# Optimization experiments

Measured on AMD Instinct MI355X. Metric: run time of the kernel, lower is better.

## Reference

```python
import jax, jax.numpy as jnp
import numpy as np

D_MODEL = 1024
D_FF = 4096
N_EXPERTS = 8
TOP_K = 2
GATE_TEMP = 1.0
LOAD_BALANCE_WEIGHT = 0.01


def setup_inputs() -> dict:
    key = jax.random.key(0)
    ks = jax.random.split(key, 6)
    B, S = 4, 2048
    x = jax.random.normal(ks[0], (B, S, D_MODEL), dtype=jnp.float32)
    # gate: nn.Linear(d_model, n_experts, bias=False), weight ~ N(0, 0.1)
    gate_w = 0.1 * jax.random.normal(ks[1], (N_EXPERTS, D_MODEL), dtype=jnp.float32)
    # stacked expert weights (stored as [in, out] for x @ W)
    s1 = 1.0 / np.sqrt(D_MODEL)
    s2 = 1.0 / np.sqrt(D_FF)
    W1 = jax.random.uniform(ks[2], (N_EXPERTS, D_MODEL, D_FF), jnp.float32, -s1, s1)
    b1 = jax.random.uniform(ks[3], (N_EXPERTS, D_FF), jnp.float32, -s1, s1)
    W2 = jax.random.uniform(ks[4], (N_EXPERTS, D_FF, D_MODEL), jnp.float32, -s2, s2)
    b2 = jax.random.uniform(ks[5], (N_EXPERTS, D_MODEL), jnp.float32, -s2, s2)
    return {"x": x, "gate_w": gate_w, "W1": W1, "b1": b1, "W2": W2, "b2": b2}


def reference(x, gate_w, W1, b1, W2, b2):
    B, S, D = x.shape
    E = gate_w.shape[0]
    xf = x.reshape(-1, D)                                  # [N, D]
    logits = (xf @ gate_w.T) / GATE_TEMP                   # [N, E]
    gate_probs = jax.nn.softmax(logits, axis=-1)           # [N, E]
    topk_probs, topk_idx = jax.lax.top_k(gate_probs, TOP_K)
    topk_probs = topk_probs / jnp.sum(topk_probs, axis=-1, keepdims=True)
    # per-token combine weight for each expert: [N, E]
    combine = jnp.einsum("nk,nke->ne", topk_probs,
                         jax.nn.one_hot(topk_idx, E, dtype=xf.dtype))
    out = jnp.zeros_like(xf)
    for e in range(E):  # fixed small loop over experts (structurally distinct weights)
        h = jax.nn.gelu(xf @ W1[e] + b1[e], approximate=False)  # [N, d_ff]
        out = out + combine[:, e:e + 1] * (h @ W2[e] + b2[e])
    out = out.reshape(B, S, D)
    # auxiliary load-balance loss (faithful: softmax probs > 0 almost surely)
    prob_mean = jnp.mean(gate_probs, axis=0)
    tokens_per_expert = jnp.mean((gate_probs > 0).astype(xf.dtype), axis=0)
    aux_loss = jnp.sum(prob_mean * tokens_per_expert) * E * LOAD_BALANCE_WEIGHT
    return out, aux_loss
```

## Files before the change

kernel.cpp:

```cpp
#include <hip/hip_runtime.h>
#include <cstdint>

typedef unsigned short u16;
typedef __attribute__((ext_vector_type(8))) __bf16 bf16x8;
typedef __attribute__((ext_vector_type(4))) float f32x4;

#define NTOK 8192
#define DM   1024
#define DFF  4096
#define NE   8
#define NT_MAX256 72

typedef const __attribute__((address_space(1))) unsigned gl_u32;
typedef __attribute__((address_space(3))) unsigned lds_u32;

static __device__ __forceinline__ u16 f2bf(float f) {
    union { float f; unsigned u; } v; v.f = f;
    unsigned r = v.u + 0x7fffu + ((v.u >> 16) & 1u);
    return (u16)(r >> 16);
}

__global__ __launch_bounds__(256) void transpose_cvt_kernel(const float* __restrict__ W,
                                                            u16* __restrict__ WT,
                                                            int K, int F) {
    __shared__ float tile[64][33];
    size_t eo = (size_t)blockIdx.z * K * F;
    const float* src = W + eo;
    u16* dst = WT + eo;
    int k0 = blockIdx.y * 64, f0 = blockIdx.x * 32;
    int tid = threadIdx.x;
    {
        int rk = tid >> 2, cf = (tid & 3) * 8;
        const float* s = src + (size_t)(k0 + rk) * F + f0 + cf;
        f32x4 v0 = *(const f32x4*)(s);
        f32x4 v1 = *(const f32x4*)(s + 4);
#pragma unroll
        for (int i = 0; i < 4; i++) { tile[rk][cf + i] = v0[i]; tile[rk][cf + 4 + i] = v1[i]; }
    }
    __syncthreads();
    {
        int f = tid >> 3, kq = (tid & 7) * 8;
        union { ushort4 h[2]; uint4 q; } o;
#pragma unroll
        for (int i = 0; i < 8; i++) {
            u16 b = f2bf(tile[kq + i][f]);
            ((u16*)&o)[i] = b;
        }
        *(uint4*)(dst + (size_t)(f0 + f) * K + k0 + kq) = o.q;
    }
}

__global__ __launch_bounds__(256) void gate_kernel(const float* __restrict__ x,
                                                   const float* __restrict__ gw,
                                                   u16* __restrict__ xb,
                                                   int* __restrict__ cnt,
                                                   float* __restrict__ psum,
                                                   float* __restrict__ indsum,
                                                   int* __restrict__ list,
                                                   float* __restrict__ wgt,
                                                   int4* __restrict__ tokIE,
                                                   float2* __restrict__ tokW) {
    __shared__ float s_psum[NE], s_ind[NE];
    __shared__ int s_cnt[NE], s_base[NE];
    __shared__ int s_tok[NE][32];
    __shared__ float s_wgt[NE][32];
    __shared__ int s_e1[32], s_p1[32], s_e2[32], s_p2[32];
    __shared__ float s_w1[32], s_w2[32];
    int tid = threadIdx.x, lane = tid & 63, wid = tid >> 6;
    if (tid < NE) { s_psum[tid] = 0.f; s_ind[tid] = 0.f; s_cnt[tid] = 0; }
    __syncthreads();
#pragma unroll 1
    for (int it = 0; it < 8; it++) {
        int t = blockIdx.x * 32 + wid * 8 + it;
        const float* xr = x + (size_t)t * DM;
        float xv[16];
#pragma unroll
        for (int i = 0; i < 4; i++) {
            f32x4 v = *(const f32x4*)(xr + i * 256 + lane * 4);
            xv[4 * i + 0] = v[0]; xv[4 * i + 1] = v[1];
            xv[4 * i + 2] = v[2]; xv[4 * i + 3] = v[3];
            ushort4 o;
            o.x = f2bf(v[0]); o.y = f2bf(v[1]); o.z = f2bf(v[2]); o.w = f2bf(v[3]);
            *(ushort4*)(xb + (size_t)t * DM + i * 256 + lane * 4) = o;
        }
        float p[NE];
#pragma unroll
        for (int e = 0; e < NE; e++) {
            const float* gr = gw + (size_t)e * DM;
            float d = 0.f;
#pragma unroll
            for (int i = 0; i < 4; i++) {
                f32x4 g = *(const f32x4*)(gr + i * 256 + lane * 4);
                d += xv[4 * i] * g[0] + xv[4 * i + 1] * g[1]
                   + xv[4 * i + 2] * g[2] + xv[4 * i + 3] * g[3];
            }
#pragma unroll
            for (int off = 32; off; off >>= 1) d += __shfl_xor(d, off);
            p[e] = d;
        }
        float m = p[0];
#pragma unroll
        for (int e = 1; e < NE; e++) m = fmaxf(m, p[e]);
        float s = 0.f;
#pragma unroll
        for (int e = 0; e < NE; e++) { p[e] = expf(p[e] - m); s += p[e]; }
        float inv = 1.f / s;
#pragma unroll
        for (int e = 0; e < NE; e++) p[e] *= inv;
        int i1 = 0; float p1 = p[0];
#pragma unroll
        for (int e = 1; e < NE; e++) if (p[e] > p1) { p1 = p[e]; i1 = e; }
        int i2 = (i1 == 0) ? 1 : 0; float p2 = p[i2];
#pragma unroll
        for (int e = 0; e < NE; e++) if (e != i1 && p[e] > p2) { p2 = p[e]; i2 = e; }
        float wnorm = 1.f / (p1 + p2);
        if (lane == 0) {
#pragma unroll
            for (int e = 0; e < NE; e++) {
                atomicAdd(&s_psum[e], p[e]);
                atomicAdd(&s_ind[e], (p[e] > 0.f) ? 1.f : 0.f);
            }
            int pos1 = atomicAdd(&s_cnt[i1], 1);
            s_tok[i1][pos1] = t; s_wgt[i1][pos1] = p1 * wnorm;
            int pos2 = atomicAdd(&s_cnt[i2], 1);
            s_tok[i2][pos2] = t; s_wgt[i2][pos2] = p2 * wnorm;
            int sl = wid * 8 + it;
            s_e1[sl] = i1; s_p1[sl] = pos1; s_w1[sl] = p1 * wnorm;
            s_e2[sl] = i2; s_p2[sl] = pos2; s_w2[sl] = p2 * wnorm;
        }
    }
    __syncthreads();
    if (tid < NE) {
        s_base[tid] = atomicAdd(&cnt[tid], s_cnt[tid]);
        atomicAdd(&psum[tid], s_psum[tid]);
        atomicAdd(&indsum[tid], s_ind[tid]);
    }
    __syncthreads();
    for (int idx = tid; idx < NE * 32; idx += 256) {
        int e = idx >> 5, j = idx & 31;
        if (j < s_cnt[e]) {
            list[e * NTOK + s_base[e] + j] = s_tok[e][j];
            wgt[e * NTOK + s_base[e] + j] = s_wgt[e][j];
        }
    }
    if (tid < 32) {
        int t = blockIdx.x * 32 + tid;
        int e1 = s_e1[tid], e2 = s_e2[tid];
        tokIE[t] = make_int4(e1, s_base[e1] + s_p1[tid], e2, s_base[e2] + s_p2[tid]);
        tokW[t] = make_float2(s_w1[tid], s_w2[tid]);
    }
}

__global__ void finalize_kernel(const float* __restrict__ psum,
                                const float* __restrict__ indsum,
                                const int* __restrict__ cnt,
                                int* __restrict__ baseArr,
                                int* __restrict__ tileE,
                                int* __restrict__ tileM0,
                                int* __restrict__ nTiles,
                                float* __restrict__ out_aux) {
    if (threadIdx.x == 0) {
        float a = 0.f; int b = 0, nt = 0;
        for (int e = 0; e < NE; e++) {
            a += (psum[e] * (1.f / NTOK)) * (indsum[e] * (1.f / NTOK));
            baseArr[e] = b; b += cnt[e];
            int mt = (cnt[e] + 255) >> 8;
            for (int i = 0; i < mt; i++) { tileE[nt] = e; tileM0[nt] = i; nt++; }
        }
        nTiles[0] = nt;
        out_aux[0] = a * (float)NE * 0.01f;
    }
}

template <int KDIM, int EPI>
__global__ __launch_bounds__(512, 2) void gemm_kernel(const u16* __restrict__ A,
                                                      const u16* __restrict__ BT,
                                                      const float* __restrict__ bias,
                                                      const int* __restrict__ list,
                                                      const float* __restrict__ wgt,
                                                      const int* __restrict__ cnt,
                                                      const int* __restrict__ base,
                                                      const int* __restrict__ tileE,
                                                      const int* __restrict__ tileM0,
                                                      const int* __restrict__ nTiles,
                                                      u16* __restrict__ h_out,
                                                      float* __restrict__ out) {
    constexpr int NCOL = (EPI == 1) ? DFF : DM;
    constexpr int NY = NCOL / 128;
    constexpr int NT = KDIM / 64;
    constexpr int BAND = 4 * NY;
    int nwg = gridDim.x;
    int q = nwg >> 3, r = nwg & 7;
    int xcd = blockIdx.x & 7, idx0 = blockIdx.x >> 3;
    int wg = (xcd < r ? xcd * (q + 1) : r * (q + 1) + (xcd - r) * q) + idx0;
    int band = wg / BAND, ib = wg - band * BAND;
    int ny = ib >> 2;
    int t = band * 4 + (ib & 3);
    if (t >= nTiles[0]) return;
    int e = tileE[t];
    int m0 = tileM0[t] << 8;
    int M = cnt[e];
    int hb = base[e];
    int n0 = ny * 128;
    const int* le = list + e * NTOK;
    const float* we = wgt + e * NTOK;
    const u16* Bte = BT + (size_t)e * NCOL * KDIM;
    const float* be = bias + (size_t)e * NCOL;

    __shared__ __attribute__((aligned(16))) u16 lA[256 * 64];
    __shared__ __attribute__((aligned(16))) u16 lB[128 * 64];

    int tid = threadIdx.x;
    int lane = tid & 63, wid = tid >> 6;
    int wm = wid >> 1, wn = wid & 1;
    int r16 = lane & 15, hi = lane >> 4;
    int r8 = r16 & 7;

    const u16* aG[4]; const u16* bG[2]; int aOfs[4], bOfs[2];
#pragma unroll
    for (int qq = 0; qq < 4; qq++) {
        int lin = qq * 512 + tid;
        int row = lin >> 3, j = lin & 7;
        int js = j ^ (row & 7);
        aOfs[qq] = lin * 8;
        int pos = m0 + row; if (pos > M - 1) pos = M - 1;
        size_t arow = (EPI == 1) ? (size_t)le[pos] : (size_t)(hb + pos);
        aG[qq] = A + arow * KDIM + js * 8;
    }
#pragma unroll
    for (int qq = 0; qq < 2; qq++) {
        int lin = qq * 512 + tid;
        int row = lin >> 3, j = lin & 7;
        int js = j ^ (row & 7);
        bOfs[qq] = lin * 8;
        bG[qq] = Bte + (size_t)(n0 + row) * KDIM + js * 8;
    }

#define STAGE(k0)                                                                   \
    do {                                                                            \
        _Pragma("unroll")                                                           \
        for (int qq = 0; qq < 4; qq++)                                              \
            __builtin_amdgcn_global_load_lds((gl_u32*)(aG[qq] + (k0)),              \
                (lds_u32*)(lA + aOfs[qq]), 16, 0, 0);                               \
        _Pragma("unroll")                                                           \
        for (int qq = 0; qq < 2; qq++)                                              \
            __builtin_amdgcn_global_load_lds((gl_u32*)(bG[qq] + (k0)),              \
                (lds_u32*)(lB + bOfs[qq]), 16, 0, 0);                               \
    } while (0)

    f32x4 acc[4][4];
#pragma unroll
    for (int m = 0; m < 4; m++)
#pragma unroll
        for (int n = 0; n < 4; n++) acc[m][n] = (f32x4){0.f, 0.f, 0.f, 0.f};

    STAGE(0);

#pragma unroll 1
    for (int tI = 0; tI < NT; ++tI) {
        asm volatile("s_waitcnt vmcnt(0)" ::: "memory");
        __builtin_amdgcn_s_barrier();
#pragma unroll
        for (int kk = 0; kk < 2; kk++) {
            bf16x8 aF[4], bF[4];
            int ch = ((kk << 2) | hi) ^ r8;
#pragma unroll
            for (int m = 0; m < 4; m++)
                aF[m] = *(const bf16x8*)(lA + ((wm * 64 + m * 16 + r16) << 6) + (ch << 3));
#pragma unroll
            for (int n = 0; n < 4; n++)
                bF[n] = *(const bf16x8*)(lB + ((wn * 64 + n * 16 + r16) << 6) + (ch << 3));
            __builtin_amdgcn_s_setprio(1);
#pragma unroll
            for (int m = 0; m < 4; m++)
#pragma unroll
                for (int n = 0; n < 4; n++)
                    acc[m][n] = __builtin_amdgcn_mfma_f32_16x16x32_bf16(aF[m], bF[n], acc[m][n], 0, 0, 0);
            __builtin_amdgcn_s_setprio(0);
        }
        asm volatile("s_waitcnt lgkmcnt(0)" ::: "memory");
        __builtin_amdgcn_s_barrier();
        if (tI + 1 < NT) STAGE((tI + 1) * 64);
    }
#undef STAGE

#pragma unroll
    for (int m = 0; m < 4; m++) {
        int pr = m0 + wm * 64 + m * 16 + hi * 4;
#pragma unroll
        for (int n = 0; n < 4; n++) {
            int f = n0 + wn * 64 + n * 16 + r16;
#pragma unroll
            for (int j = 0; j < 4; j++) {
                int p = pr + j;
                if (p < M) {
                    if constexpr (EPI == 1) {
                        float v = acc[m][n][j] + be[f];
                        float ex = __expf(v * (1.5957691216f + 0.0713548162f * v * v));
                        v = v - v / (ex + 1.0f);
                        h_out[(size_t)(hb + p) * DFF + f] = f2bf(v);
                    } else if constexpr (EPI == 2) {
                        out[(size_t)(hb + p) * DM + f] = acc[m][n][j];
                    } else {
                        atomicAdd(out + (size_t)le[p] * DM + f,
                                  we[p] * (acc[m][n][j] + be[f]));
                    }
                }
            }
        }
    }
}

__global__ __launch_bounds__(256) void combine_kernel(const float* __restrict__ pairOut,
                                                      const float* __restrict__ b2,
                                                      const int4* __restrict__ tokIE,
                                                      const float2* __restrict__ tokW,
                                                      const int* __restrict__ baseArr,
                                                      float* __restrict__ out) {
    int t = blockIdx.x;
    int c = threadIdx.x * 4;
    int4 ie = tokIE[t];
    float2 w = tokW[t];
    int s1 = baseArr[ie.x] + ie.y, s2 = baseArr[ie.z] + ie.w;
    f32x4 v1 = *(const f32x4*)(pairOut + (size_t)s1 * DM + c);
    f32x4 v2 = *(const f32x4*)(pairOut + (size_t)s2 * DM + c);
    f32x4 g1 = *(const f32x4*)(b2 + (size_t)ie.x * DM + c);
    f32x4 g2 = *(const f32x4*)(b2 + (size_t)ie.z * DM + c);
    f32x4 res = w.x * (v1 + g1) + w.y * (v2 + g2);
    *(f32x4*)(out + (size_t)t * DM + c) = res;
}

extern "C" void kernel_launch(void* const* d_in, const int* in_sizes, int n_in,
                              void* d_out, int out_size, void* d_ws, size_t ws_size,
                              hipStream_t stream) {
    const float* x  = (const float*)d_in[0];
    const float* gw = (const float*)d_in[1];
    const float* W1 = (const float*)d_in[2];
    const float* b1 = (const float*)d_in[3];
    const float* W2 = (const float*)d_in[4];
    const float* b2 = (const float*)d_in[5];
    float* out = (float*)d_out;

    char* ws = (char*)d_ws;
    size_t o_xb   = 0;
    size_t o_w1t  = (size_t)16 << 20;
    size_t o_w2t  = o_w1t + ((size_t)64 << 20);
    size_t o_h    = o_w2t + ((size_t)64 << 20);
    size_t o_pair = o_h + ((size_t)128 << 20);
    size_t ctrl_sz = (size_t)1 << 20;
    bool pair_path = ws_size >= o_pair + ((size_t)64 << 20) + ctrl_sz;
    size_t o_ctrl = pair_path ? (o_pair + ((size_t)64 << 20)) : o_pair;

    u16* xb   = (u16*)(ws + o_xb);
    u16* w1t  = (u16*)(ws + o_w1t);
    u16* w2t  = (u16*)(ws + o_w2t);
    u16* h    = (u16*)(ws + o_h);
    float* pairOut = (float*)(ws + o_pair);
    char* ctrl = ws + o_ctrl;
    int*    cnt     = (int*)ctrl;
    float*  psum    = (float*)(ctrl + 32);
    float*  indsum  = (float*)(ctrl + 64);
    int*    baseArr = (int*)(ctrl + 96);
    int*    list    = (int*)(ctrl + 192);
    float*  wgt     = (float*)(ctrl + 192 + 262144);
    int4*   tokIE   = (int4*)(ctrl + 192 + 524288);
    float2* tokW    = (float2*)(ctrl + 192 + 655360);
    int*    tileE   = (int*)(ctrl + 192 + 720896);
    int*    tileM0  = (int*)(ctrl + 192 + 724992);
    int*    nTiles  = (int*)(ctrl + 192 + 729088);

    (void)hipMemsetAsync(ctrl, 0, 192, stream);
    if (!pair_path)
        (void)hipMemsetAsync(d_out, 0, (size_t)out_size * sizeof(float), stream);

    transpose_cvt_kernel<<<dim3(DFF / 32, DM / 64, NE), 256, 0, stream>>>(W1, w1t, DM, DFF);
    transpose_cvt_kernel<<<dim3(DM / 32, DFF / 64, NE), 256, 0, stream>>>(W2, w2t, DFF, DM);
    gate_kernel<<<NTOK / 32, 256, 0, stream>>>(x, gw, xb, cnt, psum, indsum, list, wgt, tokIE, tokW);
    finalize_kernel<<<1, 64, 0, stream>>>(psum, indsum, cnt, baseArr, tileE, tileM0, nTiles,
                                          out + (size_t)NTOK * DM);

    gemm_kernel<DM, 1><<<dim3(NT_MAX256 * (DFF / 128)), 512, 0, stream>>>(
        xb, w1t, b1, list, wgt, cnt, baseArr, tileE, tileM0, nTiles, h, nullptr);
    if (pair_path) {
        gemm_kernel<DFF, 2><<<dim3(NT_MAX256 * (DM / 128)), 512, 0, stream>>>(
            h, w2t, b2, list, wgt, cnt, baseArr, tileE, tileM0, nTiles, nullptr, pairOut);
        combine_kernel<<<NTOK, 256, 0, stream>>>(pairOut, b2, tokIE, tokW, baseArr, out);
    } else {
        gemm_kernel<DFF, 3><<<dim3(NT_MAX256 * (DM / 128)), 512, 0, stream>>>(
            h, w2t, b2, list, wgt, cnt, baseArr, tileE, tileM0, nTiles, nullptr, out);
    }
}
```

Measured before the change: 572.6 us.

## Use 256x256 tiles with double-buffered quarter-tile pipelined MoE GEMM

The grouped expert GEMM moves from a 256x128 tile with a single LDS buffer to a 256x256 tile. A and B are split into 128-row halves and double-buffered in LDS. Each 64-wide K step runs as four sub-MFMA phases, and global-to-LDS loads for the next halves are issued between them, so loads overlap compute instead of stalling on a full vmcnt(0) wait each step. This raises per-wave arithmetic intensity (8x4 accumulators), at the cost of more registers, more LDS (128 KB), many more barriers and half as many workgroups.

```diff
diff --git a/kernel.cpp b/kernel.cpp
--- a/kernel.cpp
+++ b/kernel.cpp
@@ -186,8 +186,9 @@
                                                       u16* __restrict__ h_out,
                                                       float* __restrict__ out) {
     constexpr int NCOL = (EPI == 1) ? DFF : DM;
-    constexpr int NY = NCOL / 128;
+    constexpr int NY = NCOL / 256;
     constexpr int NT = KDIM / 64;
+    constexpr int NITER = NT / 2;
     constexpr int BAND = 4 * NY;
     int nwg = gridDim.x;
     int q = nwg >> 3, r = nwg & 7;
@@ -201,109 +202,142 @@
     int m0 = tileM0[t] << 8;
     int M = cnt[e];
     int hb = base[e];
-    int n0 = ny * 128;
+    int n0 = ny * 256;
     const int* le = list + e * NTOK;
     const float* we = wgt + e * NTOK;
     const u16* Bte = BT + (size_t)e * NCOL * KDIM;
     const float* be = bias + (size_t)e * NCOL;
 
-    __shared__ __attribute__((aligned(16))) u16 lA[256 * 64];
-    __shared__ __attribute__((aligned(16))) u16 lB[128 * 64];
+    __shared__ __attribute__((aligned(16))) u16 LA[2][2][128 * 64];
+    __shared__ __attribute__((aligned(16))) u16 LB[2][2][128 * 64];
 
     int tid = threadIdx.x;
     int lane = tid & 63, wid = tid >> 6;
-    int wm = wid >> 1, wn = wid & 1;
+    int wm = wid >> 2, wn = wid & 3;
     int r16 = lane & 15, hi = lane >> 4;
     int r8 = r16 & 7;
-
-    const u16* aG[4]; const u16* bG[2]; int aOfs[4], bOfs[2];
-#pragma unroll
-    for (int qq = 0; qq < 4; qq++) {
-        int lin = qq * 512 + tid;
-        int row = lin >> 3, j = lin & 7;
-        int js = j ^ (row & 7);
-        aOfs[qq] = lin * 8;
-        int pos = m0 + row; if (pos > M - 1) pos = M - 1;
-        size_t arow = (EPI == 1) ? (size_t)le[pos] : (size_t)(hb + pos);
-        aG[qq] = A + arow * KDIM + js * 8;
-    }
+    int bh = wn >> 1, brow0 = (wn & 1) * 64;
+
+    const u16* aG[2][2]; const u16* bG[2][2]; int lOfs[2];
 #pragma unroll
     for (int qq = 0; qq < 2; qq++) {
         int lin = qq * 512 + tid;
         int row = lin >> 3, j = lin & 7;
         int js = j ^ (row & 7);
-        bOfs[qq] = lin * 8;
-        bG[qq] = Bte + (size_t)(n0 + row) * KDIM + js * 8;
-    }
-
-#define STAGE(k0)                                                                   \
-    do {                                                                            \
-        _Pragma("unroll")                                                           \
-        for (int qq = 0; qq < 4; qq++)                                              \
-            __builtin_amdgcn_global_load_lds((gl_u32*)(aG[qq] + (k0)),              \
-                (lds_u32*)(lA + aOfs[qq]), 16, 0, 0);                               \
-        _Pragma("unroll")                                                           \
-        for (int qq = 0; qq < 2; qq++)                                              \
-            __builtin_amdgcn_global_load_lds((gl_u32*)(bG[qq] + (k0)),              \
-                (lds_u32*)(lB + bOfs[qq]), 16, 0, 0);                               \
+        lOfs[qq] = lin * 8;
+#pragma unroll
+        for (int ah = 0; ah < 2; ah++) {
+            int pos = m0 + ah * 128 + row; if (pos > M - 1) pos = M - 1;
+            size_t arow = (EPI == 1) ? (size_t)le[pos] : (size_t)(hb + pos);
+            aG[ah][qq] = A + arow * KDIM + js * 8;
+            bG[ah][qq] = Bte + (size_t)(n0 + ah * 128 + row) * KDIM + js * 8;
+        }
+    }
+
+#define STG_A(half, buf, k0)                                                        \
+    do { _Pragma("unroll")                                                          \
+        for (int q5 = 0; q5 < 2; q5++)                                              \
+            __builtin_amdgcn_global_load_lds((gl_u32*)(aG[half][q5] + (k0)),        \
+                (lds_u32*)(&LA[buf][half][lOfs[q5]]), 16, 0, 0);                    \
     } while (0)
-
-    f32x4 acc[4][4];
-#pragma unroll
-    for (int m = 0; m < 4; m++)
+#define STG_B(half, buf, k0)                                                        \
+    do { _Pragma("unroll")                                                          \
+        for (int q5 = 0; q5 < 2; q5++)                                              \
+            __builtin_amdgcn_global_load_lds((gl_u32*)(bG[half][q5] + (k0)),        \
+                (lds_u32*)(&LB[buf][half][lOfs[q5]]), 16, 0, 0);                    \
+    } while (0)
+#define DS_A(buf, mh)                                                               \
+    do { _Pragma("unroll")                                                          \
+        for (int i5 = 0; i5 < 4; i5++) _Pragma("unroll")                            \
+        for (int k5 = 0; k5 < 2; k5++)                                              \
+            aF[i5][k5] = *(const bf16x8*)(&LA[buf][wm][(((mh)*64 + i5*16 + r16) << 6) \
+                + ((((k5<<2)|hi)^r8) << 3)]);                                       \
+    } while (0)
+#define DS_B(buf, nh)                                                               \
+    do { _Pragma("unroll")                                                          \
+        for (int j5 = 0; j5 < 2; j5++) _Pragma("unroll")                            \
+        for (int k5 = 0; k5 < 2; k5++)                                              \
+            bF[(nh)*2+j5][k5] = *(const bf16x8*)(&LB[buf][bh][((brow0 + ((nh)*2+j5)*16 + r16) << 6) \
+                + ((((k5<<2)|hi)^r8) << 3)]);                                       \
+    } while (0)
+#define MFMAQ(mh, nh)                                                               \
+    do { __builtin_amdgcn_s_setprio(1); _Pragma("unroll")                           \
+        for (int i5 = 0; i5 < 4; i5++) _Pragma("unroll")                            \
+        for (int j5 = 0; j5 < 2; j5++) _Pragma("unroll")                            \
+        for (int k5 = 0; k5 < 2; k5++)                                              \
+            acc[(mh)*4+i5][(nh)*2+j5] = __builtin_amdgcn_mfma_f32_16x16x32_bf16(    \
+                aF[i5][k5], bF[(nh)*2+j5][k5], acc[(mh)*4+i5][(nh)*2+j5], 0, 0, 0); \
+        __builtin_amdgcn_s_setprio(0);                                              \
+    } while (0)
+#define BAR __builtin_amdgcn_s_barrier()
+#define LGK asm volatile("s_waitcnt lgkmcnt(0)" ::: "memory")
+
+    f32x4 acc[8][4];
+#pragma unroll
+    for (int m = 0; m < 8; m++)
 #pragma unroll
         for (int n = 0; n < 4; n++) acc[m][n] = (f32x4){0.f, 0.f, 0.f, 0.f};
-
-    STAGE(0);
+    bf16x8 aF[4][2], bF[4][2];
+
+    STG_A(0, 0, 0); STG_A(1, 0, 0); STG_B(0, 0, 0); STG_B(1, 0, 0);
+    STG_B(0, 1, 64); STG_B(1, 1, 64);
+    asm volatile("s_waitcnt vmcnt(4)" ::: "memory");
+    BAR;
 
 #pragma unroll 1
-    for (int tI = 0; tI < NT; ++tI) {
-        asm volatile("s_waitcnt vmcnt(0)" ::: "memory");
-        __builtin_amdgcn_s_barrier();
-#pragma unroll
-        for (int kk = 0; kk < 2; kk++) {
-            bf16x8 aF[4], bF[4];
-            int ch = ((kk << 2) | hi) ^ r8;
-#pragma unroll
-            for (int m = 0; m < 4; m++)
-                aF[m] = *(const bf16x8*)(lA + ((wm * 64 + m * 16 + r16) << 6) + (ch << 3));
-#pragma unroll
-            for (int n = 0; n < 4; n++)
-                bF[n] = *(const bf16x8*)(lB + ((wn * 64 + n * 16 + r16) << 6) + (ch << 3));
-            __builtin_amdgcn_s_setprio(1);
-#pragma unroll
-            for (int m = 0; m < 4; m++)
-#pragma unroll
-                for (int n = 0; n < 4; n++)
-                    acc[m][n] = __builtin_amdgcn_mfma_f32_16x16x32_bf16(aF[m], bF[n], acc[m][n], 0, 0, 0);
-            __builtin_amdgcn_s_setprio(0);
-        }
-        asm volatile("s_waitcnt lgkmcnt(0)" ::: "memory");
-        __builtin_amdgcn_s_barrier();
-        if (tI + 1 < NT) STAGE((tI + 1) * 64);
-    }
-#undef STAGE
-
-#pragma unroll
-    for (int m = 0; m < 4; m++) {
-        int pr = m0 + wm * 64 + m * 16 + hi * 4;
-#pragma unroll
-        for (int n = 0; n < 4; n++) {
-            int f = n0 + wn * 64 + n * 16 + r16;
+    for (int it = 0; it < NITER; ++it) {
+        int tbk = (2 * it + 1) * 64, a2k = (2 * it + 2) * 64, b2k = (2 * it + 3) * 64;
+        bool last = (it == NITER - 1);
+        DS_A(0, 0); DS_B(0, 0); STG_A(0, 1, tbk);
+        BAR; LGK; MFMAQ(0, 0); BAR;
+        DS_B(0, 1); STG_A(1, 1, tbk);
+        BAR; LGK; MFMAQ(0, 1); BAR;
+        DS_A(0, 1); if (!last) STG_B(0, 0, a2k);
+        BAR; LGK; MFMAQ(1, 1); BAR;
+        if (!last) STG_B(1, 0, a2k);
+        BAR; LGK; MFMAQ(1, 0);
+        if (last) { asm volatile("s_waitcnt vmcnt(0)" ::: "memory"); }
+        else      { asm volatile("s_waitcnt vmcnt(4)" ::: "memory"); }
+        BAR;
+        DS_A(1, 0); DS_B(1, 0); if (!last) STG_A(0, 0, a2k);
+        BAR; LGK; MFMAQ(0, 0); BAR;
+        DS_B(1, 1); if (!last) STG_A(1, 0, a2k);
+        BAR; LGK; MFMAQ(0, 1); BAR;
+        DS_A(1, 1); if (!last) STG_B(0, 1, b2k);
+        BAR; LGK; MFMAQ(1, 1); BAR;
+        if (!last) STG_B(1, 1, b2k);
+        BAR; LGK; MFMAQ(1, 0);
+        if (!last) asm volatile("s_waitcnt vmcnt(4)" ::: "memory");
+        BAR;
+    }
+#undef STG_A
+#undef STG_B
+#undef DS_A
+#undef DS_B
+#undef MFMAQ
+#undef BAR
+#undef LGK
+
+#pragma unroll
+    for (int mf = 0; mf < 8; mf++) {
+        int pr = m0 + wm * 128 + ((mf >> 2) << 6) + ((mf & 3) << 4) + hi * 4;
+#pragma unroll
+        for (int nf = 0; nf < 4; nf++) {
+            int f = n0 + wn * 64 + nf * 16 + r16;
 #pragma unroll
             for (int j = 0; j < 4; j++) {
                 int p = pr + j;
                 if (p < M) {
                     if constexpr (EPI == 1) {
-                        float v = acc[m][n][j] + be[f];
+                        float v = acc[mf][nf][j] + be[f];
                         float ex = __expf(v * (1.5957691216f + 0.0713548162f * v * v));
                         v = v - v / (ex + 1.0f);
                         h_out[(size_t)(hb + p) * DFF + f] = f2bf(v);
                     } else if constexpr (EPI == 2) {
-                        out[(size_t)(hb + p) * DM + f] = acc[m][n][j];
+                        out[(size_t)(hb + p) * DM + f] = acc[mf][nf][j];
                     } else {
                         atomicAdd(out + (size_t)le[p] * DM + f,
-                                  we[p] * (acc[m][n][j] + be[f]));
+                                  we[p] * (acc[mf][nf][j] + be[f]));
                     }
                 }
             }
@@ -379,14 +413,14 @@
     finalize_kernel<<<1, 64, 0, stream>>>(psum, indsum, cnt, baseArr, tileE, tileM0, nTiles,
                                           out + (size_t)NTOK * DM);
 
-    gemm_kernel<DM, 1><<<dim3(NT_MAX256 * (DFF / 128)), 512, 0, stream>>>(
+    gemm_kernel<DM, 1><<<dim3(NT_MAX256 * (DFF / 256)), 512, 0, stream>>>(
         xb, w1t, b1, list, wgt, cnt, baseArr, tileE, tileM0, nTiles, h, nullptr);
     if (pair_path) {
-        gemm_kernel<DFF, 2><<<dim3(NT_MAX256 * (DM / 128)), 512, 0, stream>>>(
+        gemm_kernel<DFF, 2><<<dim3(NT_MAX256 * (DM / 256)), 512, 0, stream>>>(
             h, w2t, b2, list, wgt, cnt, baseArr, tileE, tileM0, nTiles, nullptr, pairOut);
         combine_kernel<<<NTOK, 256, 0, stream>>>(pairOut, b2, tokIE, tokW, baseArr, out);
     } else {
-        gemm_kernel<DFF, 3><<<dim3(NT_MAX256 * (DM / 128)), 512, 0, stream>>>(
+        gemm_kernel<DFF, 3><<<dim3(NT_MAX256 * (DM / 256)), 512, 0, stream>>>(
             h, w2t, b2, list, wgt, cnt, baseArr, tileE, tileM0, nTiles, nullptr, out);
     }
 }
```

Result: slower. 648.9 us (+13.3%).
